# Performance work log

Hardware: AMD Instinct MI355X
Metric: run time of the kernel (lower is better)

The kernel has to match this reference:

```python
import jax, jax.numpy as jnp
import numpy as np

V = 16384      # total nodes
G = 32         # nodes per graph (512 graphs)
D = 256        # node embedding dim == hidden_size
N = 8          # heads
H = 32         # head size
I = 1024       # intermediate size
LN_EPS = 1e-12


def _layer_norm(x, g, b):
    mu = jnp.mean(x, axis=-1, keepdims=True)
    var = jnp.mean(jnp.square(x - mu), axis=-1, keepdims=True)
    return (x - mu) * jax.lax.rsqrt(var + LN_EPS) * g + b


def setup_inputs() -> dict:
    key = jax.random.key(0)
    ks = jax.random.split(key, 5)
    node_embeddings = jax.random.normal(ks[0], (V, D), jnp.float32)
    # fully-connected pairs within each graph of size G (sorted by source node)
    idx = np.arange(V, dtype=np.int32).reshape(-1, G)          # [num_graphs, G]
    src = np.repeat(idx, G, axis=1).reshape(-1)                # [P]
    dst = np.tile(idx, (1, G)).reshape(-1)                     # [P]
    in_graph_node_pairs = jnp.asarray(np.stack([src, dst], axis=-1))  # [P, 2]
    s = 0.02
    return {
        "node_embeddings": node_embeddings,
        "in_graph_node_pairs": in_graph_node_pairs,
        "W_qkv": jax.random.normal(ks[1], (D, 3 * N * H), jnp.float32) * s,
        "W_o": jax.random.normal(ks[2], (N * H, D), jnp.float32) * s,
        "ln1_g": jnp.ones((D,), jnp.float32),
        "ln1_b": jnp.zeros((D,), jnp.float32),
        "W_i": jax.random.normal(ks[3], (D, I), jnp.float32) * s,
        "W_out2": jax.random.normal(ks[4], (I, D), jnp.float32) * s,
        "ln2_g": jnp.ones((D,), jnp.float32),
        "ln2_b": jnp.zeros((D,), jnp.float32),
    }


def reference(node_embeddings, in_graph_node_pairs, W_qkv, W_o, ln1_g, ln1_b,
              W_i, W_out2, ln2_g, ln2_b):
    nV = node_embeddings.shape[0]
    src = in_graph_node_pairs[:, 0]
    dst = in_graph_node_pairs[:, 1]
    # QKV projection -> [V, N, 3H] -> split
    qkv = (node_embeddings @ W_qkv).reshape(nV, N, 3 * H)
    q, k, v = jnp.split(qkv, 3, axis=-1)                       # each [V, N, H]
    # per-pair scores [P, N]
    scores = jnp.einsum('phi,phi->ph', q[src], k[dst]) / jnp.sqrt(jnp.float32(H))
    # segment softmax over source node, all heads at once
    m = jax.ops.segment_max(scores, src, num_segments=nV)       # [V, N]
    e = jnp.exp(scores - m[src])
    denom = jax.ops.segment_sum(e, src, num_segments=nV)        # [V, N]
    w = e / denom[src]                                          # [P, N]
    # weighted value scatter-sum -> [V, N, H]
    wv = w[:, :, None] * v[dst]
    att = jax.ops.segment_sum(wv, src, num_segments=nV).reshape(nV, N * H)
    # output projection + residual + LN
    pre = _layer_norm(att @ W_o + node_embeddings, ln1_g, ln1_b)
    inter = jax.nn.gelu(pre @ W_i, approximate=False)
    out = _layer_norm(inter @ W_out2 + pre, ln2_g, ln2_b)
    return out
```

## Files before the change

kernel.cpp:

```cpp
#include <hip/hip_runtime.h>
#include <math.h>

#define V 16384
#define D 256
#define NH 256
#define THREE_NH 768
#define IDIM 1024
#define LN_EPS 1e-12f
#define SCL 0.17677669529663687f

typedef short s16x8 __attribute__((ext_vector_type(8)));
typedef float f32x4 __attribute__((ext_vector_type(4)));

__device__ inline unsigned short f2bf(float f) {
    unsigned u = __float_as_uint(f);
    u += 0x7fffu + ((u >> 16) & 1u);
    return (unsigned short)(u >> 16);
}
__device__ inline float bf2f(unsigned short s) {
    return __uint_as_float(((unsigned)s) << 16);
}

__device__ inline float fast_erf(float x) {
    float ax = fabsf(x);
    float t  = 1.f / fmaf(0.3275911f, ax, 1.f);
    float p  = fmaf(fmaf(fmaf(fmaf(1.061405429f, t, -1.453152027f), t,
                              1.421413741f), t, -0.284496736f), t, 0.254829592f);
    float e  = 1.f - p * t * __expf(-ax * ax);
    return copysignf(e, x);
}

__device__ inline void gl2lds16(const unsigned short* g, unsigned short* l) {
    __builtin_amdgcn_global_load_lds(
        (__attribute__((address_space(1))) void*)(g),
        (__attribute__((address_space(3))) void*)(l), 16, 0, 0);
}

template <int ROWS_T>
__device__ inline void stage(const unsigned short* __restrict__ src, size_t row0,
                             int ldk, int k0, unsigned short* lds, int wv, int lane) {
    constexpr int PER_WAVE = ROWS_T / 32;
    #pragma unroll
    for (int i = 0; i < PER_WAVE; ++i) {
        const int seg = wv * PER_WAVE + i;
        const int r = seg * 8 + (lane >> 3);
        const int c = (lane & 7) ^ (r & 7);
        gl2lds16(src + (row0 + (size_t)r) * ldk + k0 + c * 8, lds + seg * 512);
    }
}

__device__ inline void stage_wp(const unsigned short* __restrict__ src, size_t row0,
                                int ldk, int k0, unsigned short* seg, int lane) {
    #pragma unroll
    for (int i = 0; i < 8; ++i) {
        const int r = i * 8 + (lane >> 3);
        const int c = (lane & 7) ^ (r & 7);
        gl2lds16(src + (row0 + (size_t)r) * ldk + k0 + c * 8, seg + i * 512);
    }
}

__device__ inline s16x8 fragld(const unsigned short* lds, int row, int chunk) {
    return *(const s16x8*)&lds[row * 64 + ((chunk ^ (row & 7)) << 3)];
}

#define WAVE_LGKM0() do { asm volatile("s_waitcnt lgkmcnt(0)" ::: "memory"); \
                          __builtin_amdgcn_sched_barrier(0); } while (0)
#define WAVE_VM0()   do { asm volatile("s_waitcnt vmcnt(0)" ::: "memory");   \
                          __builtin_amdgcn_sched_barrier(0); } while (0)

__global__ __launch_bounds__(256) void prep(const float* __restrict__ X,
                                            unsigned short* __restrict__ Xb,
                                            const float* __restrict__ Wqkv,
                                            const float* __restrict__ Wo,
                                            const float* __restrict__ Wi,
                                            const float* __restrict__ Wo2,
                                            unsigned short* __restrict__ WqkvT,
                                            unsigned short* __restrict__ WoT,
                                            unsigned short* __restrict__ WiT,
                                            unsigned short* __restrict__ Wo2T) {
    const int b = blockIdx.x, t = threadIdx.x;
    if (b >= 768) {
        int i = (b - 768) * 256 + t;
        float4 v = ((const float4*)X)[i];
        ushort4 o;
        o.x = f2bf(v.x); o.y = f2bf(v.y); o.z = f2bf(v.z); o.w = f2bf(v.w);
        ((ushort4*)Xb)[i] = o;
        return;
    }
    __shared__ float tile[32][33];
    const float* W; unsigned short* Wt; int K, N, bx, by;
    if (b < 192)      { W = Wqkv; Wt = WqkvT; K = 256;  N = 768;  bx = b & 7;          by = b >> 3; }
    else if (b < 256) { W = Wo;   Wt = WoT;   K = 256;  N = 256;  bx = (b - 192) & 7;  by = (b - 192) >> 3; }
    else if (b < 512) { W = Wi;   Wt = WiT;   K = 256;  N = 1024; bx = (b - 256) & 7;  by = (b - 256) >> 3; }
    else              { W = Wo2;  Wt = Wo2T;  K = 1024; N = 256;  bx = (b - 512) & 31; by = (b - 512) >> 5; }
    const int k0 = bx * 32, n0 = by * 32;
    #pragma unroll
    for (int p = 0; p < 4; ++p) {
        int idx = t + p * 256, r = idx >> 5, c = idx & 31;
        tile[r][c] = W[(size_t)(k0 + r) * N + n0 + c];
    }
    __syncthreads();
    #pragma unroll
    for (int p = 0; p < 4; ++p) {
        int idx = t + p * 256, r = idx >> 5, c = idx & 31;
        Wt[(size_t)(n0 + r) * K + k0 + c] = f2bf(tile[c][r]);
    }
}

template <int K, int N, int EPI>
__global__ __launch_bounds__(256) void gemm128(const unsigned short* __restrict__ A,
                                               const unsigned short* __restrict__ Bt,
                                               unsigned short* __restrict__ C) {
    __shared__ unsigned short As[128 * 64];
    __shared__ unsigned short Bs[128 * 64];
    constexpr int NCOL = N / 128;
    const int b = blockIdx.x;
    const int idx = b >> 3;
    const int r0 = ((b & 7) * 16 + idx / NCOL) * 128;
    const int c0 = (idx % NCOL) * 128;
    const int t = threadIdx.x;
    const int wv = t >> 6, lane = t & 63, q = lane >> 4, l16 = lane & 15;
    const int wr = (wv >> 1) * 64, wc = (wv & 1) * 64;
    f32x4 acc[4][4] = {};

    for (int k0 = 0; k0 < K; k0 += 64) {
        __syncthreads();
        stage<128>(A,  (size_t)r0, K, k0, As, wv, lane);
        stage<128>(Bt, (size_t)c0, K, k0, Bs, wv, lane);
        __builtin_amdgcn_s_waitcnt(0);
        __syncthreads();
        #pragma unroll
        for (int kk2 = 0; kk2 < 2; ++kk2) {
            s16x8 af[4], bfr[4];
            #pragma unroll
            for (int mf = 0; mf < 4; ++mf)
                af[mf] = fragld(As, wr + mf * 16 + l16, kk2 * 4 + q);
            #pragma unroll
            for (int nf = 0; nf < 4; ++nf)
                bfr[nf] = fragld(Bs, wc + nf * 16 + l16, kk2 * 4 + q);
            #pragma unroll
            for (int mf = 0; mf < 4; ++mf)
                #pragma unroll
                for (int nf = 0; nf < 4; ++nf)
                    acc[mf][nf] = __builtin_amdgcn_mfma_f32_16x16x32_bf16(af[mf], bfr[nf], acc[mf][nf], 0, 0, 0);
        }
    }

    #pragma unroll
    for (int mf = 0; mf < 4; ++mf)
        #pragma unroll
        for (int nf = 0; nf < 4; ++nf) {
            const int cg = c0 + wc + nf * 16 + l16;
            #pragma unroll
            for (int r = 0; r < 4; ++r) {
                const int rg = r0 + wr + mf * 16 + q * 4 + r;
                float v = acc[mf][nf][r];
                if (EPI == 1) v = 0.5f * v * (1.f + fast_erf(v * 0.70710678118654752f));
                C[(size_t)rg * N + cg] = f2bf(v);
            }
        }
}

__global__ __launch_bounds__(256) void ffn_ln(const unsigned short* __restrict__ preb,
                                              const unsigned short* __restrict__ WiT,
                                              const unsigned short* __restrict__ Wo2T,
                                              const float* __restrict__ gamma,
                                              const float* __restrict__ beta,
                                              float* __restrict__ out) {
    __shared__ unsigned short Apre[8192];
    __shared__ unsigned short Bs[16384];
    __shared__ unsigned short Pbuf[8192];
    __shared__ float2 partial[4][32];
    __shared__ float2 stats[32];
    const int t = threadIdx.x, r0 = blockIdx.x * 32;
    const int wv = t >> 6, lane = t & 63, q = lane >> 4, l16 = lane & 15;
    const int wc = wv * 64;
    unsigned short* Bseg = Bs + wv * 4096;
    f32x4 acc2[2][4] = {};

    #pragma unroll
    for (int kc = 0; kc < 4; ++kc)
        stage<32>(preb, (size_t)r0, 256, kc * 64, Apre + kc * 2048, wv, lane);
    __builtin_amdgcn_s_waitcnt(0);
    __syncthreads();

    for (int nc = 0; nc < 4; ++nc) {
        f32x4 acc1[2][4] = {};
        #pragma unroll
        for (int k0 = 0; k0 < 256; k0 += 64) {
            WAVE_LGKM0();
            stage_wp(WiT, (size_t)(nc * 256 + wc), 256, k0, Bseg, lane);
            WAVE_VM0();
            const unsigned short* Ak = Apre + (k0 >> 6) * 2048;
            #pragma unroll
            for (int kk2 = 0; kk2 < 2; ++kk2) {
                s16x8 af[2], bv[4];
                #pragma unroll
                for (int mf = 0; mf < 2; ++mf)
                    af[mf] = fragld(Ak, mf * 16 + l16, kk2 * 4 + q);
                #pragma unroll
                for (int nf = 0; nf < 4; ++nf)
                    bv[nf] = fragld(Bseg, nf * 16 + l16, kk2 * 4 + q);
                #pragma unroll
                for (int mf = 0; mf < 2; ++mf)
                    #pragma unroll
                    for (int nf = 0; nf < 4; ++nf)
                        acc1[mf][nf] = __builtin_amdgcn_mfma_f32_16x16x32_bf16(af[mf], bv[nf], acc1[mf][nf], 0, 0, 0);
            }
        }

        #pragma unroll
        for (int mf = 0; mf < 2; ++mf)
            #pragma unroll
            for (int nf = 0; nf < 4; ++nf)
                #pragma unroll
                for (int r = 0; r < 4; ++r) {
                    float v = acc1[mf][nf][r];
                    v = 0.5f * v * (1.f + fast_erf(v * 0.70710678118654752f));
                    const int i = mf * 16 + q * 4 + r;
                    const int colc = wc + nf * 16 + l16;
                    const int c8 = (colc >> 3) & 7;
                    Pbuf[wv * 2048 + i * 64 + ((c8 ^ (i & 7)) << 3) + (colc & 7)] = f2bf(v);
                }
        __syncthreads();

        #pragma unroll
        for (int ks = 0; ks < 256; ks += 64) {
            WAVE_LGKM0();
            stage_wp(Wo2T, (size_t)wc, IDIM, nc * 256 + ks, Bseg, lane);
            WAVE_VM0();
            const unsigned short* Pk = Pbuf + (ks >> 6) * 2048;
            #pragma unroll
            for (int kk2 = 0; kk2 < 2; ++kk2) {
                s16x8 af[2], bv[4];
                #pragma unroll
                for (int mf = 0; mf < 2; ++mf)
                    af[mf] = fragld(Pk, mf * 16 + l16, kk2 * 4 + q);
                #pragma unroll
                for (int nf = 0; nf < 4; ++nf)
                    bv[nf] = fragld(Bseg, nf * 16 + l16, kk2 * 4 + q);
                #pragma unroll
                for (int mf = 0; mf < 2; ++mf)
                    #pragma unroll
                    for (int nf = 0; nf < 4; ++nf)
                        acc2[mf][nf] = __builtin_amdgcn_mfma_f32_16x16x32_bf16(af[mf], bv[nf], acc2[mf][nf], 0, 0, 0);
            }
        }
        __syncthreads();
    }

    #pragma unroll
    for (int mf = 0; mf < 2; ++mf)
        #pragma unroll
        for (int nf = 0; nf < 4; ++nf) {
            const int cg = wc + nf * 16 + l16;
            const int kb = cg >> 6, c8 = (cg >> 3) & 7, e = cg & 7;
            #pragma unroll
            for (int r = 0; r < 4; ++r) {
                const int i = mf * 16 + q * 4 + r;
                acc2[mf][nf][r] += bf2f(Apre[kb * 2048 + i * 64 + ((c8 ^ (i & 7)) << 3) + e]);
            }
        }

    #pragma unroll
    for (int mf = 0; mf < 2; ++mf) {
        float s[4] = {0.f, 0.f, 0.f, 0.f}, ss[4] = {0.f, 0.f, 0.f, 0.f};
        #pragma unroll
        for (int nf = 0; nf < 4; ++nf)
            #pragma unroll
            for (int r = 0; r < 4; ++r) {
                float v = acc2[mf][nf][r];
                s[r] += v; ss[r] += v * v;
            }
        #pragma unroll
        for (int off = 1; off < 16; off <<= 1)
            #pragma unroll
            for (int r = 0; r < 4; ++r) {
                s[r]  += __shfl_xor(s[r],  off);
                ss[r] += __shfl_xor(ss[r], off);
            }
        if (l16 == 0)
            #pragma unroll
            for (int r = 0; r < 4; ++r)
                partial[wv][mf * 16 + q * 4 + r] = make_float2(s[r], ss[r]);
    }
    __syncthreads();
    if (t < 32) {
        float s = 0.f, ss = 0.f;
        #pragma unroll
        for (int w = 0; w < 4; ++w) { s += partial[w][t].x; ss += partial[w][t].y; }
        float mu  = s * (1.f / 256.f);
        float var = ss * (1.f / 256.f) - mu * mu;
        stats[t] = make_float2(mu, rsqrtf(var + LN_EPS));
    }
    __syncthreads();

    #pragma unroll
    for (int mf = 0; mf < 2; ++mf)
        #pragma unroll
        for (int nf = 0; nf < 4; ++nf) {
            const int cg = wc + nf * 16 + l16;
            const float g = gamma[cg], b = beta[cg];
            #pragma unroll
            for (int r = 0; r < 4; ++r) {
                const int rl = mf * 16 + q * 4 + r;
                const float2 st = stats[rl];
                out[(size_t)(r0 + rl) * NH + cg] = (acc2[mf][nf][r] - st.x) * st.y * g + b;
            }
        }
}

__global__ __launch_bounds__(256) void attln(const unsigned short* __restrict__ qkv,
                                             const unsigned short* __restrict__ WoT,
                                             const float* __restrict__ X,
                                             const float* __restrict__ gamma,
                                             const float* __restrict__ beta,
                                             unsigned short* __restrict__ preb) {
    __shared__ unsigned short smem[25216];
    unsigned short* Ks = smem;
    unsigned short* Vt = smem + 8192;
    unsigned short* Ps = smem + 16384;
    unsigned short* at = smem;
    unsigned short* Bs = smem + 8192;
    float2* partial = (float2*)(smem + 24576);
    float2* stats   = (float2*)(smem + 24576 + 512);

    const int g = blockIdx.x, t = threadIdx.x;
    const int wv = t >> 6, lane = t & 63, q = lane >> 4, l16 = lane & 15;
    const unsigned short* src = qkv + (size_t)g * 32 * THREE_NH;

    s16x8 qf[2][2];
    #pragma unroll
    for (int hh = 0; hh < 2; ++hh)
        #pragma unroll
        for (int mf = 0; mf < 2; ++mf)
            qf[hh][mf] = *(const s16x8*)&src[(size_t)(mf * 16 + l16) * THREE_NH +
                                             (wv * 2 + hh) * 96 + q * 8];

    s16x8 vld[4];
    int vh[4], vj[4], vdc[4];
    #pragma unroll
    for (int i = 0; i < 4; ++i) {
        int cid = i * 256 + t;
        vh[i] = cid >> 7; int rem = cid & 127; vj[i] = rem >> 2; vdc[i] = rem & 3;
        vld[i] = *(const s16x8*)&src[(size_t)vj[i] * THREE_NH + vh[i] * 96 + 64 + vdc[i] * 8];
    }

    #pragma unroll
    for (int i = 0; i < 4; ++i) {
        int ck = (wv * 4 + i) * 64 + lane;
        int h = ck >> 7, j = (ck >> 2) & 31, c = ck & 3;
        gl2lds16(src + (size_t)j * THREE_NH + h * 96 + 32 + c * 8, Ks + (wv * 4 + i) * 512);
    }

    #pragma unroll
    for (int i = 0; i < 4; ++i)
        #pragma unroll
        for (int e = 0; e < 8; ++e) {
            int d = vdc[i] * 8 + e;
            Vt[vh[i] * 1024 + d * 32 + ((((vj[i] >> 3) ^ ((d >> 2) & 3))) << 3) + (vj[i] & 7)] =
                (unsigned short)vld[i][e];
        }

    __builtin_amdgcn_s_waitcnt(0);
    __syncthreads();

    f32x4 sacc[2][2][2] = {};
    #pragma unroll
    for (int hh = 0; hh < 2; ++hh) {
        const int h = wv * 2 + hh;
        #pragma unroll
        for (int nf = 0; nf < 2; ++nf) {
            s16x8 kf = *(const s16x8*)&Ks[h * 1024 + (nf * 16 + l16) * 32 + q * 8];
            #pragma unroll
            for (int mf = 0; mf < 2; ++mf)
                sacc[hh][mf][nf] = __builtin_amdgcn_mfma_f32_16x16x32_bf16(
                    qf[hh][mf], kf, sacc[hh][mf][nf], 0, 0, 0);
        }
    }

    float inv[2][2][4];
    #pragma unroll
    for (int hh = 0; hh < 2; ++hh) {
        const int h = wv * 2 + hh;
        #pragma unroll
        for (int mf = 0; mf < 2; ++mf)
            #pragma unroll
            for (int r = 0; r < 4; ++r) {
                float a0 = sacc[hh][mf][0][r], a1 = sacc[hh][mf][1][r];
                float m = fmaxf(a0, a1);
                m = fmaxf(m, __shfl_xor(m, 1));
                m = fmaxf(m, __shfl_xor(m, 2));
                m = fmaxf(m, __shfl_xor(m, 4));
                m = fmaxf(m, __shfl_xor(m, 8));
                float e0 = __expf((a0 - m) * SCL);
                float e1 = __expf((a1 - m) * SCL);
                float sm = e0 + e1;
                sm += __shfl_xor(sm, 1);
                sm += __shfl_xor(sm, 2);
                sm += __shfl_xor(sm, 4);
                sm += __shfl_xor(sm, 8);
                inv[hh][mf][r] = 1.f / sm;
                const int row = mf * 16 + q * 4 + r;
                const int base = h * 1024 + row * 32 + (l16 & 7);
                Ps[base + ((((l16 >> 3) ^ q)) << 3)]       = f2bf(e0);
                Ps[base + ((((2 + (l16 >> 3)) ^ q)) << 3)] = f2bf(e1);
            }
    }

    f32x4 oacc[2][2][2] = {};
    #pragma unroll
    for (int hh = 0; hh < 2; ++hh) {
        const int h = wv * 2 + hh;
        const int sw = (l16 >> 2) & 3;
        s16x8 pa[2], vb[2];
        #pragma unroll
        for (int mf = 0; mf < 2; ++mf)
            pa[mf] = *(const s16x8*)&Ps[h * 1024 + (mf * 16 + l16) * 32 + ((q ^ sw) << 3)];
        #pragma unroll
        for (int nf = 0; nf < 2; ++nf)
            vb[nf] = *(const s16x8*)&Vt[h * 1024 + (nf * 16 + l16) * 32 + ((q ^ sw) << 3)];
        #pragma unroll
        for (int mf = 0; mf < 2; ++mf)
            #pragma unroll
            for (int nf = 0; nf < 2; ++nf)
                oacc[hh][mf][nf] = __builtin_amdgcn_mfma_f32_16x16x32_bf16(
                    pa[mf], vb[nf], oacc[hh][mf][nf], 0, 0, 0);
    }
    __syncthreads();

    #pragma unroll
    for (int hh = 0; hh < 2; ++hh)
        #pragma unroll
        for (int mf = 0; mf < 2; ++mf)
            #pragma unroll
            for (int nf = 0; nf < 2; ++nf)
                #pragma unroll
                for (int r = 0; r < 4; ++r) {
                    float val = oacc[hh][mf][nf][r] * inv[hh][mf][r];
                    const int i = mf * 16 + q * 4 + r;
                    const int col = (wv * 2 + hh) * 32 + nf * 16 + l16;
                    const int kb = col >> 6, c = (col >> 3) & 7;
                    at[kb * 2048 + i * 64 + ((c ^ (i & 7)) << 3) + (col & 7)] = f2bf(val);
                }
    __syncthreads();

    const int wc = wv * 64;
    const int r0 = g * 32;
    unsigned short* Bseg = Bs + wv * 4096;
    f32x4 acc[2][4] = {};

    #pragma unroll
    for (int kc = 0; kc < 4; ++kc) {
        WAVE_LGKM0();
        stage_wp(WoT, (size_t)wc, 256, kc * 64, Bseg, lane);
        WAVE_VM0();
        const unsigned short* atk = at + kc * 2048;
        #pragma unroll
        for (int kk2 = 0; kk2 < 2; ++kk2) {
            s16x8 af[2], bv[4];
            #pragma unroll
            for (int mf = 0; mf < 2; ++mf)
                af[mf] = fragld(atk, mf * 16 + l16, kk2 * 4 + q);
            #pragma unroll
            for (int nf = 0; nf < 4; ++nf)
                bv[nf] = fragld(Bseg, nf * 16 + l16, kk2 * 4 + q);
            #pragma unroll
            for (int mf = 0; mf < 2; ++mf)
                #pragma unroll
                for (int nf = 0; nf < 4; ++nf)
                    acc[mf][nf] = __builtin_amdgcn_mfma_f32_16x16x32_bf16(af[mf], bv[nf], acc[mf][nf], 0, 0, 0);
        }
    }

    #pragma unroll
    for (int mf = 0; mf < 2; ++mf)
        #pragma unroll
        for (int nf = 0; nf < 4; ++nf) {
            const int cg = wc + nf * 16 + l16;
            #pragma unroll
            for (int r = 0; r < 4; ++r)
                acc[mf][nf][r] += X[(size_t)(r0 + mf * 16 + q * 4 + r) * NH + cg];
        }

    #pragma unroll
    for (int mf = 0; mf < 2; ++mf) {
        float sp[4] = {0.f, 0.f, 0.f, 0.f}, ssp[4] = {0.f, 0.f, 0.f, 0.f};
        #pragma unroll
        for (int nf = 0; nf < 4; ++nf)
            #pragma unroll
            for (int r = 0; r < 4; ++r) {
                float v = acc[mf][nf][r];
                sp[r] += v; ssp[r] += v * v;
            }
        #pragma unroll
        for (int off = 1; off < 16; off <<= 1)
            #pragma unroll
            for (int r = 0; r < 4; ++r) {
                sp[r]  += __shfl_xor(sp[r],  off);
                ssp[r] += __shfl_xor(ssp[r], off);
            }
        if (l16 == 0)
            #pragma unroll
            for (int r = 0; r < 4; ++r)
                partial[wv * 32 + mf * 16 + q * 4 + r] = make_float2(sp[r], ssp[r]);
    }
    __syncthreads();
    if (t < 32) {
        float sv = 0.f, ssv = 0.f;
        #pragma unroll
        for (int w = 0; w < 4; ++w) { sv += partial[w * 32 + t].x; ssv += partial[w * 32 + t].y; }
        float mu  = sv * (1.f / 256.f);
        float var = ssv * (1.f / 256.f) - mu * mu;
        stats[t] = make_float2(mu, rsqrtf(var + LN_EPS));
    }
    __syncthreads();

    #pragma unroll
    for (int mf = 0; mf < 2; ++mf)
        #pragma unroll
        for (int nf = 0; nf < 4; ++nf) {
            const int cg = wc + nf * 16 + l16;
            const float gm = gamma[cg], bt = beta[cg];
            #pragma unroll
            for (int r = 0; r < 4; ++r) {
                const int rl = mf * 16 + q * 4 + r;
                const float2 st = stats[rl];
                float v = (acc[mf][nf][r] - st.x) * st.y * gm + bt;
                preb[(size_t)(r0 + rl) * NH + cg] = f2bf(v);
            }
        }
}

extern "C" void kernel_launch(void* const* d_in, const int* in_sizes, int n_in,
                              void* d_out, int out_size, void* d_ws, size_t ws_size,
                              hipStream_t stream) {
    const float* X      = (const float*)d_in[0];
    const float* W_qkv  = (const float*)d_in[2];
    const float* W_o    = (const float*)d_in[3];
    const float* ln1_g  = (const float*)d_in[4];
    const float* ln1_b  = (const float*)d_in[5];
    const float* W_i    = (const float*)d_in[6];
    const float* W_out2 = (const float*)d_in[7];
    const float* ln2_g  = (const float*)d_in[8];
    const float* ln2_b  = (const float*)d_in[9];
    float* out = (float*)d_out;

    char* ws = (char*)d_ws;
    unsigned short* Xbf   = (unsigned short*)(ws);
    unsigned short* qkvb  = (unsigned short*)(ws + 8388608);
    unsigned short* preb  = (unsigned short*)(ws + 58720256);
    unsigned short* WqkvT = (unsigned short*)(ws + 67108864);
    unsigned short* WoT   = (unsigned short*)(ws + 67502080);
    unsigned short* WiT   = (unsigned short*)(ws + 67633152);
    unsigned short* Wo2T  = (unsigned short*)(ws + 68157440);

    dim3 blk(256);
    hipLaunchKernelGGL(prep, dim3(768 + V * D / 4 / 256), blk, 0, stream,
                       X, Xbf, W_qkv, W_o, W_i, W_out2, WqkvT, WoT, WiT, Wo2T);

    hipLaunchKernelGGL((gemm128<D, THREE_NH, 0>), dim3(V / 128 * (THREE_NH / 128)), blk, 0, stream,
                       Xbf, WqkvT, qkvb);
    hipLaunchKernelGGL(attln, dim3(V / 32), blk, 0, stream,
                       qkvb, WoT, X, ln1_g, ln1_b, preb);
    hipLaunchKernelGGL(ffn_ln, dim3(V / 32), blk, 0, stream,
                       preb, WiT, Wo2T, ln2_g, ln2_b, out);
}
```

Baseline: 153.7 us.

## Widen FFN block to 64 rows with shared double-buffered weight tiles

The fused FFN+LayerNorm kernel now runs 512 threads on 64 rows per block instead of 256 threads on 32 rows. The 8 waves form a 2x4 grid and share one 256x64 weight tile in LDS, rather than each wave staging its own slice. Each weight tile is now loaded once per 64 rows, which halves weight traffic per row, and the next K tile is prefetched into a second buffer during the MFMAs. The cost is 128 KB of LDS per block, which limits occupancy to one block per CU, plus a full-block barrier on every K step.

```diff
diff --git a/kernel.cpp b/kernel.cpp
--- a/kernel.cpp
+++ b/kernel.cpp
@@ -40,6 +40,19 @@
 __device__ inline void stage(const unsigned short* __restrict__ src, size_t row0,
                              int ldk, int k0, unsigned short* lds, int wv, int lane) {
     constexpr int PER_WAVE = ROWS_T / 32;
+    #pragma unroll
+    for (int i = 0; i < PER_WAVE; ++i) {
+        const int seg = wv * PER_WAVE + i;
+        const int r = seg * 8 + (lane >> 3);
+        const int c = (lane & 7) ^ (r & 7);
+        gl2lds16(src + (row0 + (size_t)r) * ldk + k0 + c * 8, lds + seg * 512);
+    }
+}
+
+template <int ROWS_T>
+__device__ inline void stage8(const unsigned short* __restrict__ src, size_t row0,
+                              int ldk, int k0, unsigned short* lds, int wv, int lane) {
+    constexpr int PER_WAVE = ROWS_T / 64;
     #pragma unroll
     for (int i = 0; i < PER_WAVE; ++i) {
         const int seg = wv * PER_WAVE + i;
@@ -161,52 +174,59 @@
         }
 }
 
-__global__ __launch_bounds__(256) void ffn_ln(const unsigned short* __restrict__ preb,
+__global__ __launch_bounds__(512) void ffn_ln(const unsigned short* __restrict__ preb,
                                               const unsigned short* __restrict__ WiT,
                                               const unsigned short* __restrict__ Wo2T,
                                               const float* __restrict__ gamma,
                                               const float* __restrict__ beta,
                                               float* __restrict__ out) {
-    __shared__ unsigned short Apre[8192];
-    __shared__ unsigned short Bs[16384];
-    __shared__ unsigned short Pbuf[8192];
-    __shared__ float2 partial[4][32];
-    __shared__ float2 stats[32];
-    const int t = threadIdx.x, r0 = blockIdx.x * 32;
+    __shared__ unsigned short smem[65536];
+    unsigned short* Apre = smem;
+    unsigned short* BsA  = smem + 16384;
+    unsigned short* BsB  = smem + 32768;
+    unsigned short* Pbuf = smem + 49152;
+    float2* partial = (float2*)(smem + 49152);
+    float2* stats   = (float2*)(smem + 49152 + 1024);
+
+    const int t = threadIdx.x, r0 = blockIdx.x * 64;
     const int wv = t >> 6, lane = t & 63, q = lane >> 4, l16 = lane & 15;
-    const int wc = wv * 64;
-    unsigned short* Bseg = Bs + wv * 4096;
+    const int wm = wv >> 2, wn = wv & 3;
+    const int rbase = wm * 32, cbase = wn * 64;
     f32x4 acc2[2][4] = {};
 
     #pragma unroll
     for (int kc = 0; kc < 4; ++kc)
-        stage<32>(preb, (size_t)r0, 256, kc * 64, Apre + kc * 2048, wv, lane);
-    __builtin_amdgcn_s_waitcnt(0);
-    __syncthreads();
+        stage8<64>(preb, (size_t)r0, 256, kc * 64, Apre + kc * 4096, wv, lane);
 
     for (int nc = 0; nc < 4; ++nc) {
         f32x4 acc1[2][4] = {};
-        #pragma unroll
-        for (int k0 = 0; k0 < 256; k0 += 64) {
-            WAVE_LGKM0();
-            stage_wp(WiT, (size_t)(nc * 256 + wc), 256, k0, Bseg, lane);
-            WAVE_VM0();
-            const unsigned short* Ak = Apre + (k0 >> 6) * 2048;
+        stage8<256>(WiT, (size_t)nc * 256, 256, 0, BsA, wv, lane);
+        __builtin_amdgcn_s_waitcnt(0);
+        __syncthreads();
+        #pragma unroll
+        for (int k0 = 0; k0 < 4; ++k0) {
+            const unsigned short* cur = (k0 & 1) ? BsB : BsA;
+            if (k0 < 3)
+                stage8<256>(WiT, (size_t)nc * 256, 256, (k0 + 1) * 64,
+                            (k0 & 1) ? BsA : BsB, wv, lane);
+            const unsigned short* Ak = Apre + k0 * 4096;
             #pragma unroll
             for (int kk2 = 0; kk2 < 2; ++kk2) {
                 s16x8 af[2], bv[4];
                 #pragma unroll
                 for (int mf = 0; mf < 2; ++mf)
-                    af[mf] = fragld(Ak, mf * 16 + l16, kk2 * 4 + q);
+                    af[mf] = fragld(Ak, rbase + mf * 16 + l16, kk2 * 4 + q);
                 #pragma unroll
                 for (int nf = 0; nf < 4; ++nf)
-                    bv[nf] = fragld(Bseg, nf * 16 + l16, kk2 * 4 + q);
+                    bv[nf] = fragld(cur, cbase + nf * 16 + l16, kk2 * 4 + q);
                 #pragma unroll
                 for (int mf = 0; mf < 2; ++mf)
                     #pragma unroll
                     for (int nf = 0; nf < 4; ++nf)
                         acc1[mf][nf] = __builtin_amdgcn_mfma_f32_16x16x32_bf16(af[mf], bv[nf], acc1[mf][nf], 0, 0, 0);
             }
+            __builtin_amdgcn_s_waitcnt(0);
+            __syncthreads();
         }
 
         #pragma unroll
@@ -217,48 +237,52 @@
                 for (int r = 0; r < 4; ++r) {
                     float v = acc1[mf][nf][r];
                     v = 0.5f * v * (1.f + fast_erf(v * 0.70710678118654752f));
-                    const int i = mf * 16 + q * 4 + r;
-                    const int colc = wc + nf * 16 + l16;
-                    const int c8 = (colc >> 3) & 7;
-                    Pbuf[wv * 2048 + i * 64 + ((c8 ^ (i & 7)) << 3) + (colc & 7)] = f2bf(v);
+                    const int i = rbase + mf * 16 + q * 4 + r;
+                    const int c = cbase + nf * 16 + l16;
+                    Pbuf[(c >> 6) * 4096 + i * 64 + ((((c >> 3) & 7) ^ (i & 7)) << 3) + (c & 7)] = f2bf(v);
                 }
         __syncthreads();
 
-        #pragma unroll
-        for (int ks = 0; ks < 256; ks += 64) {
-            WAVE_LGKM0();
-            stage_wp(Wo2T, (size_t)wc, IDIM, nc * 256 + ks, Bseg, lane);
-            WAVE_VM0();
-            const unsigned short* Pk = Pbuf + (ks >> 6) * 2048;
+        stage8<256>(Wo2T, 0, IDIM, nc * 256, BsA, wv, lane);
+        __builtin_amdgcn_s_waitcnt(0);
+        __syncthreads();
+        #pragma unroll
+        for (int ks = 0; ks < 4; ++ks) {
+            const unsigned short* cur = (ks & 1) ? BsB : BsA;
+            if (ks < 3)
+                stage8<256>(Wo2T, 0, IDIM, nc * 256 + (ks + 1) * 64,
+                            (ks & 1) ? BsA : BsB, wv, lane);
+            const unsigned short* Pk = Pbuf + ks * 4096;
             #pragma unroll
             for (int kk2 = 0; kk2 < 2; ++kk2) {
                 s16x8 af[2], bv[4];
                 #pragma unroll
                 for (int mf = 0; mf < 2; ++mf)
-                    af[mf] = fragld(Pk, mf * 16 + l16, kk2 * 4 + q);
+                    af[mf] = fragld(Pk, rbase + mf * 16 + l16, kk2 * 4 + q);
                 #pragma unroll
                 for (int nf = 0; nf < 4; ++nf)
-                    bv[nf] = fragld(Bseg, nf * 16 + l16, kk2 * 4 + q);
+                    bv[nf] = fragld(cur, cbase + nf * 16 + l16, kk2 * 4 + q);
                 #pragma unroll
                 for (int mf = 0; mf < 2; ++mf)
                     #pragma unroll
                     for (int nf = 0; nf < 4; ++nf)
                         acc2[mf][nf] = __builtin_amdgcn_mfma_f32_16x16x32_bf16(af[mf], bv[nf], acc2[mf][nf], 0, 0, 0);
             }
-        }
-        __syncthreads();
+            __builtin_amdgcn_s_waitcnt(0);
+            __syncthreads();
+        }
     }
 
     #pragma unroll
     for (int mf = 0; mf < 2; ++mf)
         #pragma unroll
         for (int nf = 0; nf < 4; ++nf) {
-            const int cg = wc + nf * 16 + l16;
+            const int cg = cbase + nf * 16 + l16;
             const int kb = cg >> 6, c8 = (cg >> 3) & 7, e = cg & 7;
             #pragma unroll
             for (int r = 0; r < 4; ++r) {
-                const int i = mf * 16 + q * 4 + r;
-                acc2[mf][nf][r] += bf2f(Apre[kb * 2048 + i * 64 + ((c8 ^ (i & 7)) << 3) + e]);
+                const int i = rbase + mf * 16 + q * 4 + r;
+                acc2[mf][nf][r] += bf2f(Apre[kb * 4096 + i * 64 + ((c8 ^ (i & 7)) << 3) + e]);
             }
         }
 
@@ -282,13 +306,13 @@
         if (l16 == 0)
             #pragma unroll
             for (int r = 0; r < 4; ++r)
-                partial[wv][mf * 16 + q * 4 + r] = make_float2(s[r], ss[r]);
-    }
-    __syncthreads();
-    if (t < 32) {
+                partial[wn * 64 + rbase + mf * 16 + q * 4 + r] = make_float2(s[r], ss[r]);
+    }
+    __syncthreads();
+    if (t < 64) {
         float s = 0.f, ss = 0.f;
         #pragma unroll
-        for (int w = 0; w < 4; ++w) { s += partial[w][t].x; ss += partial[w][t].y; }
+        for (int w = 0; w < 4; ++w) { s += partial[w * 64 + t].x; ss += partial[w * 64 + t].y; }
         float mu  = s * (1.f / 256.f);
         float var = ss * (1.f / 256.f) - mu * mu;
         stats[t] = make_float2(mu, rsqrtf(var + LN_EPS));
@@ -299,13 +323,13 @@
     for (int mf = 0; mf < 2; ++mf)
         #pragma unroll
         for (int nf = 0; nf < 4; ++nf) {
-            const int cg = wc + nf * 16 + l16;
+            const int cg = cbase + nf * 16 + l16;
             const float g = gamma[cg], b = beta[cg];
             #pragma unroll
             for (int r = 0; r < 4; ++r) {
-                const int rl = mf * 16 + q * 4 + r;
-                const float2 st = stats[rl];
-                out[(size_t)(r0 + rl) * NH + cg] = (acc2[mf][nf][r] - st.x) * st.y * g + b;
+                const int i = rbase + mf * 16 + q * 4 + r;
+                const float2 st = stats[i];
+                out[(size_t)(r0 + i) * NH + cg] = (acc2[mf][nf][r] - st.x) * st.y * g + b;
             }
         }
 }
@@ -563,6 +587,6 @@
                        Xbf, WqkvT, qkvb);
     hipLaunchKernelGGL(attln, dim3(V / 32), blk, 0, stream,
                        qkvb, WoT, X, ln1_g, ln1_b, preb);
-    hipLaunchKernelGGL(ffn_ln, dim3(V / 32), blk, 0, stream,
+    hipLaunchKernelGGL(ffn_ln, dim3(V / 64), dim3(512), 0, stream,
                        preb, WiT, Wo2T, ln2_g, ln2_b, out);
 }
```

After: 159.7 us. 1.04x slower.

## Prefetch next weight tile early to hide global loads behind epilogues

Applied to the files above, without the earlier changes.

The per-wave weight tile loads are moved so each is issued right after the current chunk's MFMA work, instead of just before it. The load of the next stage's first tile is issued before the GELU epilogue, the block barriers and the attention output write, so its latency overlaps that work. The same change is made in the attention kernel's output projection, where the first W_o tile is issued before the attention results are written to LDS. The buffer is still single, so within the k-loops the load latency is only partly hidden. The MFMA inner loop is also factored into a helper function.

```diff
diff --git a/kernel.cpp b/kernel.cpp
--- a/kernel.cpp
+++ b/kernel.cpp
@@ -161,6 +161,25 @@
         }
 }
 
+__device__ inline void ffn_mfma8(const unsigned short* At, const unsigned short* Bb,
+                                 int l16, int q, f32x4 (&acc)[2][4]) {
+    #pragma unroll
+    for (int kk2 = 0; kk2 < 2; ++kk2) {
+        s16x8 af[2], bv[4];
+        #pragma unroll
+        for (int mf = 0; mf < 2; ++mf)
+            af[mf] = fragld(At, mf * 16 + l16, kk2 * 4 + q);
+        #pragma unroll
+        for (int nf = 0; nf < 4; ++nf)
+            bv[nf] = fragld(Bb, nf * 16 + l16, kk2 * 4 + q);
+        #pragma unroll
+        for (int mf = 0; mf < 2; ++mf)
+            #pragma unroll
+            for (int nf = 0; nf < 4; ++nf)
+                acc[mf][nf] = __builtin_amdgcn_mfma_f32_16x16x32_bf16(af[mf], bv[nf], acc[mf][nf], 0, 0, 0);
+    }
+}
+
 __global__ __launch_bounds__(256) void ffn_ln(const unsigned short* __restrict__ preb,
                                               const unsigned short* __restrict__ WiT,
                                               const unsigned short* __restrict__ Wo2T,
@@ -181,32 +200,23 @@
     #pragma unroll
     for (int kc = 0; kc < 4; ++kc)
         stage<32>(preb, (size_t)r0, 256, kc * 64, Apre + kc * 2048, wv, lane);
+    stage_wp(WiT, (size_t)wc, 256, 0, Bseg, lane);
     __builtin_amdgcn_s_waitcnt(0);
     __syncthreads();
 
     for (int nc = 0; nc < 4; ++nc) {
+        const int ncn = (nc + 1) & 3;
         f32x4 acc1[2][4] = {};
+
         #pragma unroll
         for (int k0 = 0; k0 < 256; k0 += 64) {
+            WAVE_VM0();
+            ffn_mfma8(Apre + (k0 >> 6) * 2048, Bseg, l16, q, acc1);
             WAVE_LGKM0();
-            stage_wp(WiT, (size_t)(nc * 256 + wc), 256, k0, Bseg, lane);
-            WAVE_VM0();
-            const unsigned short* Ak = Apre + (k0 >> 6) * 2048;
-            #pragma unroll
-            for (int kk2 = 0; kk2 < 2; ++kk2) {
-                s16x8 af[2], bv[4];
-                #pragma unroll
-                for (int mf = 0; mf < 2; ++mf)
-                    af[mf] = fragld(Ak, mf * 16 + l16, kk2 * 4 + q);
-                #pragma unroll
-                for (int nf = 0; nf < 4; ++nf)
-                    bv[nf] = fragld(Bseg, nf * 16 + l16, kk2 * 4 + q);
-                #pragma unroll
-                for (int mf = 0; mf < 2; ++mf)
-                    #pragma unroll
-                    for (int nf = 0; nf < 4; ++nf)
-                        acc1[mf][nf] = __builtin_amdgcn_mfma_f32_16x16x32_bf16(af[mf], bv[nf], acc1[mf][nf], 0, 0, 0);
-            }
+            if (k0 < 192)
+                stage_wp(WiT, (size_t)(nc * 256 + wc), 256, k0 + 64, Bseg, lane);
+            else
+                stage_wp(Wo2T, (size_t)wc, IDIM, nc * 256, Bseg, lane);
         }
 
         #pragma unroll
@@ -226,25 +236,13 @@
 
         #pragma unroll
         for (int ks = 0; ks < 256; ks += 64) {
+            WAVE_VM0();
+            ffn_mfma8(Pbuf + (ks >> 6) * 2048, Bseg, l16, q, acc2);
             WAVE_LGKM0();
-            stage_wp(Wo2T, (size_t)wc, IDIM, nc * 256 + ks, Bseg, lane);
-            WAVE_VM0();
-            const unsigned short* Pk = Pbuf + (ks >> 6) * 2048;
-            #pragma unroll
-            for (int kk2 = 0; kk2 < 2; ++kk2) {
-                s16x8 af[2], bv[4];
-                #pragma unroll
-                for (int mf = 0; mf < 2; ++mf)
-                    af[mf] = fragld(Pk, mf * 16 + l16, kk2 * 4 + q);
-                #pragma unroll
-                for (int nf = 0; nf < 4; ++nf)
-                    bv[nf] = fragld(Bseg, nf * 16 + l16, kk2 * 4 + q);
-                #pragma unroll
-                for (int mf = 0; mf < 2; ++mf)
-                    #pragma unroll
-                    for (int nf = 0; nf < 4; ++nf)
-                        acc2[mf][nf] = __builtin_amdgcn_mfma_f32_16x16x32_bf16(af[mf], bv[nf], acc2[mf][nf], 0, 0, 0);
-            }
+            if (ks < 192)
+                stage_wp(Wo2T, (size_t)wc, IDIM, nc * 256 + ks + 64, Bseg, lane);
+            else
+                stage_wp(WiT, (size_t)(ncn * 256 + wc), 256, 0, Bseg, lane);
         }
         __syncthreads();
     }
@@ -429,6 +427,10 @@
     }
     __syncthreads();
 
+    const int wc = wv * 64;
+    unsigned short* Bseg = Bs + wv * 4096;
+    stage_wp(WoT, (size_t)wc, 256, 0, Bseg, lane);
+
     #pragma unroll
     for (int hh = 0; hh < 2; ++hh)
         #pragma unroll
@@ -445,15 +447,11 @@
                 }
     __syncthreads();
 
-    const int wc = wv * 64;
     const int r0 = g * 32;
-    unsigned short* Bseg = Bs + wv * 4096;
     f32x4 acc[2][4] = {};
 
     #pragma unroll
     for (int kc = 0; kc < 4; ++kc) {
-        WAVE_LGKM0();
-        stage_wp(WoT, (size_t)wc, 256, kc * 64, Bseg, lane);
         WAVE_VM0();
         const unsigned short* atk = at + kc * 2048;
         #pragma unroll
@@ -470,6 +468,10 @@
                 #pragma unroll
                 for (int nf = 0; nf < 4; ++nf)
                     acc[mf][nf] = __builtin_amdgcn_mfma_f32_16x16x32_bf16(af[mf], bv[nf], acc[mf][nf], 0, 0, 0);
+        }
+        if (kc < 3) {
+            WAVE_LGKM0();
+            stage_wp(WoT, (size_t)wc, 256, (kc + 1) * 64, Bseg, lane);
         }
     }
 
```

Result: no change. 153.7 us (+0.0%).
